# Kernel optimization log

Measured on AMD Instinct MI355X. Metric: run time of the kernel, lower is better.

## Reference

```python
import jax, jax.numpy as jnp
import numpy as np

INPUT_DIM = 64
INNER_DIM = 64
BATCH = 32768


def setup_inputs() -> dict:
    key = jax.random.key(0)
    ks = jax.random.split(key, 9)
    D, I = INPUT_DIM, INNER_DIM
    s1 = 1.0  # Linear(1, inner): fan_in=1
    s2 = 1.0 / np.sqrt(I)
    sg1 = 1.0 / np.sqrt(D * I)
    sg2 = 1.0 / np.sqrt(I)
    return {
        "x": jax.random.normal(ks[0], (BATCH, D), dtype=jnp.float32),
        # per-feature psi params, stacked over feature dim D
        "W1": jax.random.uniform(ks[1], (D, I), jnp.float32, -s1, s1),   # Linear(1, inner) weight
        "b1": jax.random.uniform(ks[2], (D, I), jnp.float32, -s1, s1),
        "W2": jax.random.uniform(ks[3], (D, I, I), jnp.float32, -s2, s2),  # Linear(inner, inner)
        "b2": jax.random.uniform(ks[4], (D, I), jnp.float32, -s2, s2),
        # g params
        "Wg1": jax.random.uniform(ks[5], (D * I, I), jnp.float32, -sg1, sg1),
        "bg1": jax.random.uniform(ks[6], (I,), jnp.float32, -sg1, sg1),
        "Wg2": jax.random.uniform(ks[7], (I, 1), jnp.float32, -sg2, sg2),
        "bg2": jax.random.uniform(ks[8], (1,), jnp.float32, -sg2, sg2),
    }


def reference(x, W1, b1, W2, b2, Wg1, bg1, Wg2, bg2):
    B = x.shape[0]
    # all psi_i first layers as one broadcasted outer product: [B, D, I]
    h = jnp.tanh(x[:, :, None] * W1[None, :, :] + b1[None, :, :])
    # per-feature second Linear(inner, inner): batched matmul over D
    psi = jnp.einsum("bdi,dio->bdo", h, W2) + b2[None, :, :]
    psi_concat = psi.reshape(B, -1)  # [B, D*I] == torch.cat over features
    hg = jnp.tanh(psi_concat @ Wg1 + bg1)
    out = hg @ Wg2 + bg2  # [B, 1]
    return out
```

## Files before the change

### kernel.cpp

```cpp
#include <hip/hip_runtime.h>
#include <stdint.h>

#define BATCH 32768
#define TANH_C 2.8853900817779268f

typedef __attribute__((ext_vector_type(8))) short short8;
typedef __attribute__((ext_vector_type(4))) float f32x4;
typedef __attribute__((ext_vector_type(4))) unsigned int u32x4;

__device__ __forceinline__ uint16_t bf16_rtne(float f) {
    union { float f; uint32_t u; } v; v.f = f;
    uint32_t u = v.u;
    u += 0x7fffu + ((u >> 16) & 1u);
    return (uint16_t)(u >> 16);
}

#if defined(__has_builtin)
#if __has_builtin(__builtin_amdgcn_cvt_pk_bf16_f32)
#define HAVE_CVT_PK_BF16 1
#endif
#endif

__device__ __forceinline__ uint32_t pack2_bf16(float a, float b) {
#ifdef HAVE_CVT_PK_BF16
    auto v = __builtin_amdgcn_cvt_pk_bf16_f32(a, b);
    uint32_t r; __builtin_memcpy(&r, &v, 4); return r;
#else
    return (uint32_t)bf16_rtne(a) | ((uint32_t)bf16_rtne(b) << 16);
#endif
}

__device__ __forceinline__ float tanh_pre(float a) {
    float e = __builtin_amdgcn_exp2f(a);
    return 1.0f - 2.0f * __builtin_amdgcn_rcpf(1.0f + e);
}

__device__ __forceinline__ float fast_tanh(float x) {
    return tanh_pre(x * TANH_C);
}

__global__ __launch_bounds__(512) void kol_pack(const float* __restrict__ W2,
                                                const float* __restrict__ Wg1,
                                                const float* __restrict__ b2,
                                                uint16_t* __restrict__ Bp,
                                                float* __restrict__ cgpart) {
    __shared__ __align__(16) float w2t[64 * 65];
    __shared__ __align__(16) float g1s[64 * 64];

    const int t = threadIdx.x;
    const int d = blockIdx.x;

    for (int f = t * 4; f < 4096; f += 2048) {
        float4 v = *(const float4*)&W2[(size_t)d * 4096 + f];
        int j = f >> 6, o = f & 63;
        w2t[(o + 0) * 65 + j] = v.x;
        w2t[(o + 1) * 65 + j] = v.y;
        w2t[(o + 2) * 65 + j] = v.z;
        w2t[(o + 3) * 65 + j] = v.w;
        *(float4*)&g1s[f] = *(const float4*)&Wg1[(size_t)d * 4096 + f];
    }
    __syncthreads();

    const int jg = t >> 6;
    const int n  = t & 63;
    float acc[8];
#pragma unroll
    for (int i = 0; i < 8; ++i) acc[i] = 0.f;

#pragma unroll 4
    for (int o = 0; o < 64; ++o) {
        float g = g1s[o * 64 + n];
        const float* w = &w2t[o * 65 + jg * 8];
#pragma unroll
        for (int jj = 0; jj < 8; ++jj) acc[jj] = fmaf(w[jj], g, acc[jj]);
    }

    u32x4 pk;
    pk.x = pack2_bf16(acc[0], acc[1]);
    pk.y = pack2_bf16(acc[2], acc[3]);
    pk.z = pack2_bf16(acc[4], acc[5]);
    pk.w = pack2_bf16(acc[6], acc[7]);
    int off = ((d * 2 + (jg >> 2)) * 4 + (n >> 4)) * 64 + (jg & 3) * 16 + (n & 15);
    ((u32x4*)Bp)[off] = pk;

    if (t < 64) {
        float a = 0.f;
        const float* b2d = &b2[(size_t)d * 64];
#pragma unroll 4
        for (int o = 0; o < 64; ++o)
            a = fmaf(b2d[o], g1s[o * 64 + t], a);
        cgpart[d * 64 + t] = a;
    }
}

__global__ __launch_bounds__(256) void kol_reduce_cg(const float* __restrict__ cgpart,
                                                     const float* __restrict__ bg1,
                                                     float* __restrict__ cg) {
    __shared__ float red[4][64];
    const int t = threadIdx.x;
    const int n = t & 63, seg = t >> 6;
    float a = 0.f;
#pragma unroll 4
    for (int d = seg * 16; d < seg * 16 + 16; ++d)
        a += cgpart[d * 64 + n];
    red[seg][n] = a;
    __syncthreads();
    if (t < 64)
        cg[n] = bg1[n] + red[0][n] + red[1][n] + red[2][n] + red[3][n];
}

__global__ __launch_bounds__(512, 2) void kol_main(
    const float* __restrict__ x, const float* __restrict__ W1, const float* __restrict__ b1,
    const uint16_t* __restrict__ Bp, const float* __restrict__ cg,
    const float* __restrict__ Wg2, const float* __restrict__ bg2f,
    float* __restrict__ out) {
    __shared__ __align__(16) float xs[128 * 68];
    __shared__ __align__(16) float w1s[4096];
    __shared__ __align__(16) float b1s[4096];

    const int tid = threadIdx.x;
    const int wave = tid >> 6, lane = tid & 63;
    const int quad = lane >> 4, lm = lane & 15;
    const int rowbase = blockIdx.x * 128;

    for (int f = tid * 4; f < 8192; f += 2048) {
        int r = f >> 6, c = f & 63;
        float4 v = *(const float4*)&x[(size_t)(rowbase + r) * 64 + c];
        v.x *= TANH_C; v.y *= TANH_C; v.z *= TANH_C; v.w *= TANH_C;
        *(float4*)&xs[r * 68 + c] = v;
    }
    for (int f = tid * 4; f < 4096; f += 2048) {
        *(float4*)&w1s[f] = *(const float4*)&W1[f];
        float4 b = *(const float4*)&b1[f];
        b.x *= TANH_C; b.y *= TANH_C; b.z *= TANH_C; b.w *= TANH_C;
        *(float4*)&b1s[f] = b;
    }
    __syncthreads();

    f32x4 acc[4];
#pragma unroll
    for (int nt = 0; nt < 4; ++nt) acc[nt] = (f32x4){0.f, 0.f, 0.f, 0.f};

    const int myrow = wave * 16 + lm;
    const float* xrow = &xs[myrow * 68];
    const short8* bbase = (const short8*)Bp + lane;

    short8 bf[8];
#pragma unroll
    for (int i = 0; i < 8; ++i) bf[i] = bbase[i * 64];

#pragma unroll 2
    for (int d = 0; d < 64; ++d) {
        short8 bn[8];
        const short8* bpn = bbase + (size_t)((d + 1) & 63) * 512;
#pragma unroll
        for (int i = 0; i < 8; ++i) bn[i] = bpn[i * 64];

        const float xv = xrow[d];
        const float* wq = &w1s[d * 64 + quad * 8];
        const float* bq = &b1s[d * 64 + quad * 8];
        float4 wA = *(const float4*)&wq[0];
        float4 wB = *(const float4*)&wq[4];
        float4 wC = *(const float4*)&wq[32];
        float4 wD = *(const float4*)&wq[36];
        float4 bA = *(const float4*)&bq[0];
        float4 bB = *(const float4*)&bq[4];
        float4 bC = *(const float4*)&bq[32];
        float4 bD = *(const float4*)&bq[36];

        union { short8 s; uint32_t u[4]; } a0, a1;
        a0.u[0] = pack2_bf16(tanh_pre(fmaf(xv, wA.x, bA.x)), tanh_pre(fmaf(xv, wA.y, bA.y)));
        a0.u[1] = pack2_bf16(tanh_pre(fmaf(xv, wA.z, bA.z)), tanh_pre(fmaf(xv, wA.w, bA.w)));
        a0.u[2] = pack2_bf16(tanh_pre(fmaf(xv, wB.x, bB.x)), tanh_pre(fmaf(xv, wB.y, bB.y)));
        a0.u[3] = pack2_bf16(tanh_pre(fmaf(xv, wB.z, bB.z)), tanh_pre(fmaf(xv, wB.w, bB.w)));
        a1.u[0] = pack2_bf16(tanh_pre(fmaf(xv, wC.x, bC.x)), tanh_pre(fmaf(xv, wC.y, bC.y)));
        a1.u[1] = pack2_bf16(tanh_pre(fmaf(xv, wC.z, bC.z)), tanh_pre(fmaf(xv, wC.w, bC.w)));
        a1.u[2] = pack2_bf16(tanh_pre(fmaf(xv, wD.x, bD.x)), tanh_pre(fmaf(xv, wD.y, bD.y)));
        a1.u[3] = pack2_bf16(tanh_pre(fmaf(xv, wD.z, bD.z)), tanh_pre(fmaf(xv, wD.w, bD.w)));

#pragma unroll
        for (int nt = 0; nt < 4; ++nt)
            acc[nt] = __builtin_amdgcn_mfma_f32_16x16x32_bf16(a0.s, bf[nt], acc[nt], 0, 0, 0);
#pragma unroll
        for (int nt = 0; nt < 4; ++nt)
            acc[nt] = __builtin_amdgcn_mfma_f32_16x16x32_bf16(a1.s, bf[4 + nt], acc[nt], 0, 0, 0);

#pragma unroll
        for (int i = 0; i < 8; ++i) bf[i] = bn[i];
    }

    float wg2v[4], cgv[4];
#pragma unroll
    for (int nt = 0; nt < 4; ++nt) {
        wg2v[nt] = Wg2[nt * 16 + lm];
        cgv[nt]  = cg[nt * 16 + lm];
    }
    const float bg2 = bg2f[0];
#pragma unroll
    for (int r = 0; r < 4; ++r) {
        float s = 0.f;
#pragma unroll
        for (int nt = 0; nt < 4; ++nt)
            s += wg2v[nt] * fast_tanh(acc[nt][r] + cgv[nt]);
        s += __shfl_xor(s, 1, 64);
        s += __shfl_xor(s, 2, 64);
        s += __shfl_xor(s, 4, 64);
        s += __shfl_xor(s, 8, 64);
        if (lm == 0) {
            int row = rowbase + wave * 16 + quad * 4 + r;
            out[row] = s + bg2;
        }
    }
}

extern "C" void kernel_launch(void* const* d_in, const int* in_sizes, int n_in,
                              void* d_out, int out_size, void* d_ws, size_t ws_size,
                              hipStream_t stream) {
    const float* x   = (const float*)d_in[0];
    const float* W1  = (const float*)d_in[1];
    const float* b1  = (const float*)d_in[2];
    const float* W2  = (const float*)d_in[3];
    const float* b2  = (const float*)d_in[4];
    const float* Wg1 = (const float*)d_in[5];
    const float* bg1 = (const float*)d_in[6];
    const float* Wg2 = (const float*)d_in[7];
    const float* bg2 = (const float*)d_in[8];
    float* out = (float*)d_out;

    uint16_t* Bp   = (uint16_t*)d_ws;
    float* cg      = (float*)((char*)d_ws + 4096 * 64 * 2);
    float* cgpart  = out;

    kol_pack<<<64, 512, 0, stream>>>(W2, Wg1, b2, Bp, cgpart);
    kol_reduce_cg<<<1, 256, 0, stream>>>(cgpart, bg1, cg);
    kol_main<<<BATCH / 128, 512, 0, stream>>>(x, W1, b1, Bp, cg, Wg2, bg2, out);
}
```

Baseline: 129.8 us.

## Split K across wave halves and pair tanh reciprocals in main kernel

The main kernel now handles 64 rows per block. The eight waves split the 64 features into two halves, and partial accumulators are combined through shared memory before the epilogue. This doubles the grid and raises the occupancy hint to 4 blocks per CU, to hide latency. Separately, the tanh evaluation shares one reciprocal between two values, which saves transcendental throughput at the cost of a few extra multiplies and possible overflow or precision risk when the product of the denominators gets large.

```diff
diff --git a/kernel.cpp b/kernel.cpp
--- a/kernel.cpp
+++ b/kernel.cpp
@@ -30,13 +30,19 @@
 #endif
 }
 
-__device__ __forceinline__ float tanh_pre(float a) {
-    float e = __builtin_amdgcn_exp2f(a);
+__device__ __forceinline__ uint32_t tanh2_pack(float a, float b) {
+    float ea = __builtin_amdgcn_exp2f(a);
+    float eb = __builtin_amdgcn_exp2f(b);
+    float da = 1.0f + ea, db = 1.0f + eb;
+    float ir = __builtin_amdgcn_rcpf(da * db);
+    float ha = fmaf(-2.0f * db, ir, 1.0f);
+    float hb = fmaf(-2.0f * da, ir, 1.0f);
+    return pack2_bf16(ha, hb);
+}
+
+__device__ __forceinline__ float fast_tanh(float x) {
+    float e = __builtin_amdgcn_exp2f(x * TANH_C);
     return 1.0f - 2.0f * __builtin_amdgcn_rcpf(1.0f + e);
-}
-
-__device__ __forceinline__ float fast_tanh(float x) {
-    return tanh_pre(x * TANH_C);
 }
 
 __global__ __launch_bounds__(512) void kol_pack(const float* __restrict__ W2,
@@ -109,27 +115,28 @@
         cg[n] = bg1[n] + red[0][n] + red[1][n] + red[2][n] + red[3][n];
 }
 
-__global__ __launch_bounds__(512, 2) void kol_main(
+__global__ __launch_bounds__(512, 4) void kol_main(
     const float* __restrict__ x, const float* __restrict__ W1, const float* __restrict__ b1,
     const uint16_t* __restrict__ Bp, const float* __restrict__ cg,
     const float* __restrict__ Wg2, const float* __restrict__ bg2f,
     float* __restrict__ out) {
-    __shared__ __align__(16) float xs[128 * 68];
+    __shared__ __align__(16) float xs[64 * 68];
     __shared__ __align__(16) float w1s[4096];
     __shared__ __align__(16) float b1s[4096];
 
     const int tid = threadIdx.x;
     const int wave = tid >> 6, lane = tid & 63;
     const int quad = lane >> 4, lm = lane & 15;
-    const int rowbase = blockIdx.x * 128;
-
-    for (int f = tid * 4; f < 8192; f += 2048) {
+    const int w4 = wave & 3, kh = wave >> 2;
+    const int rowbase = blockIdx.x * 64;
+
+#pragma unroll
+    for (int ff = 0; ff < 2; ++ff) {
+        int f = tid * 4 + ff * 2048;
         int r = f >> 6, c = f & 63;
         float4 v = *(const float4*)&x[(size_t)(rowbase + r) * 64 + c];
         v.x *= TANH_C; v.y *= TANH_C; v.z *= TANH_C; v.w *= TANH_C;
         *(float4*)&xs[r * 68 + c] = v;
-    }
-    for (int f = tid * 4; f < 4096; f += 2048) {
         *(float4*)&w1s[f] = *(const float4*)&W1[f];
         float4 b = *(const float4*)&b1[f];
         b.x *= TANH_C; b.y *= TANH_C; b.z *= TANH_C; b.w *= TANH_C;
@@ -141,18 +148,23 @@
 #pragma unroll
     for (int nt = 0; nt < 4; ++nt) acc[nt] = (f32x4){0.f, 0.f, 0.f, 0.f};
 
-    const int myrow = wave * 16 + lm;
+    const int dlo = kh * 32;
+    const int myrow = w4 * 16 + lm;
     const float* xrow = &xs[myrow * 68];
     const short8* bbase = (const short8*)Bp + lane;
 
     short8 bf[8];
-#pragma unroll
-    for (int i = 0; i < 8; ++i) bf[i] = bbase[i * 64];
+    {
+        const short8* bp0 = bbase + (size_t)dlo * 512;
+#pragma unroll
+        for (int i = 0; i < 8; ++i) bf[i] = bp0[i * 64];
+    }
 
 #pragma unroll 2
-    for (int d = 0; d < 64; ++d) {
+    for (int dd = 0; dd < 32; ++dd) {
+        const int d = dlo + dd;
         short8 bn[8];
-        const short8* bpn = bbase + (size_t)((d + 1) & 63) * 512;
+        const short8* bpn = bbase + (size_t)(dlo + ((dd + 1) & 31)) * 512;
 #pragma unroll
         for (int i = 0; i < 8; ++i) bn[i] = bpn[i * 64];
 
@@ -169,14 +181,14 @@
         float4 bD = *(const float4*)&bq[36];
 
         union { short8 s; uint32_t u[4]; } a0, a1;
-        a0.u[0] = pack2_bf16(tanh_pre(fmaf(xv, wA.x, bA.x)), tanh_pre(fmaf(xv, wA.y, bA.y)));
-        a0.u[1] = pack2_bf16(tanh_pre(fmaf(xv, wA.z, bA.z)), tanh_pre(fmaf(xv, wA.w, bA.w)));
-        a0.u[2] = pack2_bf16(tanh_pre(fmaf(xv, wB.x, bB.x)), tanh_pre(fmaf(xv, wB.y, bB.y)));
-        a0.u[3] = pack2_bf16(tanh_pre(fmaf(xv, wB.z, bB.z)), tanh_pre(fmaf(xv, wB.w, bB.w)));
-        a1.u[0] = pack2_bf16(tanh_pre(fmaf(xv, wC.x, bC.x)), tanh_pre(fmaf(xv, wC.y, bC.y)));
-        a1.u[1] = pack2_bf16(tanh_pre(fmaf(xv, wC.z, bC.z)), tanh_pre(fmaf(xv, wC.w, bC.w)));
-        a1.u[2] = pack2_bf16(tanh_pre(fmaf(xv, wD.x, bD.x)), tanh_pre(fmaf(xv, wD.y, bD.y)));
-        a1.u[3] = pack2_bf16(tanh_pre(fmaf(xv, wD.z, bD.z)), tanh_pre(fmaf(xv, wD.w, bD.w)));
+        a0.u[0] = tanh2_pack(fmaf(xv, wA.x, bA.x), fmaf(xv, wA.y, bA.y));
+        a0.u[1] = tanh2_pack(fmaf(xv, wA.z, bA.z), fmaf(xv, wA.w, bA.w));
+        a0.u[2] = tanh2_pack(fmaf(xv, wB.x, bB.x), fmaf(xv, wB.y, bB.y));
+        a0.u[3] = tanh2_pack(fmaf(xv, wB.z, bB.z), fmaf(xv, wB.w, bB.w));
+        a1.u[0] = tanh2_pack(fmaf(xv, wC.x, bC.x), fmaf(xv, wC.y, bC.y));
+        a1.u[1] = tanh2_pack(fmaf(xv, wC.z, bC.z), fmaf(xv, wC.w, bC.w));
+        a1.u[2] = tanh2_pack(fmaf(xv, wD.x, bD.x), fmaf(xv, wD.y, bD.y));
+        a1.u[3] = tanh2_pack(fmaf(xv, wD.z, bD.z), fmaf(xv, wD.w, bD.w));
 
 #pragma unroll
         for (int nt = 0; nt < 4; ++nt)
@@ -189,26 +201,43 @@
         for (int i = 0; i < 8; ++i) bf[i] = bn[i];
     }
 
-    float wg2v[4], cgv[4];
-#pragma unroll
-    for (int nt = 0; nt < 4; ++nt) {
-        wg2v[nt] = Wg2[nt * 16 + lm];
-        cgv[nt]  = cg[nt * 16 + lm];
-    }
-    const float bg2 = bg2f[0];
-#pragma unroll
-    for (int r = 0; r < 4; ++r) {
-        float s = 0.f;
-#pragma unroll
-        for (int nt = 0; nt < 4; ++nt)
-            s += wg2v[nt] * fast_tanh(acc[nt][r] + cgv[nt]);
-        s += __shfl_xor(s, 1, 64);
-        s += __shfl_xor(s, 2, 64);
-        s += __shfl_xor(s, 4, 64);
-        s += __shfl_xor(s, 8, 64);
-        if (lm == 0) {
-            int row = rowbase + wave * 16 + quad * 4 + r;
-            out[row] = s + bg2;
+    __syncthreads();
+    float* cmb = xs;
+    if (kh == 1) {
+        int cb = (w4 * 64 + lane) * 17;
+#pragma unroll
+        for (int nt = 0; nt < 4; ++nt) *(f32x4*)&cmb[cb + nt * 4] = acc[nt];
+    }
+    __syncthreads();
+
+    if (kh == 0) {
+        int cb = (w4 * 64 + lane) * 17;
+#pragma unroll
+        for (int nt = 0; nt < 4; ++nt) {
+            f32x4 o = *(const f32x4*)&cmb[cb + nt * 4];
+            acc[nt] = acc[nt] + o;
+        }
+        float wg2v[4], cgv[4];
+#pragma unroll
+        for (int nt = 0; nt < 4; ++nt) {
+            wg2v[nt] = Wg2[nt * 16 + lm];
+            cgv[nt]  = cg[nt * 16 + lm];
+        }
+        const float bg2 = bg2f[0];
+#pragma unroll
+        for (int r = 0; r < 4; ++r) {
+            float s = 0.f;
+#pragma unroll
+            for (int nt = 0; nt < 4; ++nt)
+                s += wg2v[nt] * fast_tanh(acc[nt][r] + cgv[nt]);
+            s += __shfl_xor(s, 1, 64);
+            s += __shfl_xor(s, 2, 64);
+            s += __shfl_xor(s, 4, 64);
+            s += __shfl_xor(s, 8, 64);
+            if (lm == 0) {
+                int row = rowbase + w4 * 16 + quad * 4 + r;
+                out[row] = s + bg2;
+            }
         }
     }
 }
@@ -227,11 +256,11 @@
     const float* bg2 = (const float*)d_in[8];
     float* out = (float*)d_out;
 
-    uint16_t* Bp   = (uint16_t*)d_ws;
-    float* cg      = (float*)((char*)d_ws + 4096 * 64 * 2);
-    float* cgpart  = out;
+    uint16_t* Bp  = (uint16_t*)d_ws;
+    float* cg     = (float*)((char*)d_ws + 4096 * 64 * 2);
+    float* cgpart = out;
 
     kol_pack<<<64, 512, 0, stream>>>(W2, Wg1, b2, Bp, cgpart);
     kol_reduce_cg<<<1, 256, 0, stream>>>(cgpart, bg1, cg);
-    kol_main<<<BATCH / 128, 512, 0, stream>>>(x, W1, b1, Bp, cg, Wg2, bg2, out);
-}
+    kol_main<<<BATCH / 64, 512, 0, stream>>>(x, W1, b1, Bp, cg, Wg2, bg2, out);
+}
```

New measurement: 126.9 us. -2.2%, faster.
